# Optimization experiments

Measured on AMD Instinct MI355X. Metric: run time of the kernel, lower is better.

The kernel has to match this reference:

```python
import jax, jax.numpy as jnp
import numpy as np

EMBED = 512
WINDOW = 64

def setup_inputs() -> dict:
    key = jax.random.key(0)
    ks = jax.random.split(key, 5)
    B, S, E = 4, 4096, EMBED
    s = 1.0 / np.sqrt(E)
    x = jax.random.normal(ks[0], (B, S, E), dtype=jnp.float32)
    W_qkv = jax.random.uniform(ks[1], (E, 3 * E), minval=-s, maxval=s, dtype=jnp.float32)
    b_qkv = jax.random.uniform(ks[2], (3 * E,), minval=-s, maxval=s, dtype=jnp.float32)
    W_out = jax.random.uniform(ks[3], (E, E), minval=-s, maxval=s, dtype=jnp.float32)
    b_out = jax.random.uniform(ks[4], (E,), minval=-s, maxval=s, dtype=jnp.float32)
    return {"x": x, "W_qkv": W_qkv, "b_qkv": b_qkv, "W_out": W_out, "b_out": b_out}

def reference(x, W_qkv, b_qkv, W_out, b_out):
    B, S, E = x.shape
    scale = jnp.sqrt(jnp.asarray(E, dtype=x.dtype))
    qkv = x @ W_qkv + b_qkv                    # [B,S,3E]
    q, k, v = jnp.split(qkv, 3, axis=-1)       # each [B,S,E]
    scores = jnp.einsum('bqe,bke->bqk', q, k) / scale  # [B,S,S]
    pos = jnp.arange(S)
    dist = pos[None, :] - pos[:, None]         # [S,S]
    window_mask = jnp.abs(dist) <= WINDOW
    neg_inf = jnp.asarray(-jnp.inf, dtype=scores.dtype)
    scores = jnp.where(window_mask[None, :, :], scores, neg_inf)
    attn = jax.nn.softmax(scores, axis=-1)     # every row has in-window entries
    attended = jnp.einsum('bqk,bke->bqe', attn, v)
    return attended @ W_out + b_out
```

## Files before the change

### kernel.cpp

```cpp
#include <hip/hip_runtime.h>

typedef __attribute__((ext_vector_type(8))) _Float16 f16x8;
typedef __attribute__((ext_vector_type(4))) _Float16 f16x4;
typedef __attribute__((ext_vector_type(4))) float f32x4;
typedef __attribute__((address_space(1))) const char gc_char;
typedef __attribute__((address_space(3))) char ls_char;

#define MFMA(a, b, c) __builtin_amdgcn_mfma_f32_16x16x32_f16((a), (b), (c), 0, 0, 0)
#define FENCE() asm volatile("" ::: "memory")
#define BARRIER() do { FENCE(); __builtin_amdgcn_s_barrier(); FENCE(); } while (0)
#define VMW(n) asm volatile("s_waitcnt vmcnt(" #n ")" ::: "memory")

static constexpr int SEQ = 4096;
static constexpr int EMB = 512;
static constexpr float QSCALE = 0.04419417382415922f;

__device__ __forceinline__ void gl_lds16(const void* g, void* l) {
    __builtin_amdgcn_global_load_lds((gc_char*)g, (ls_char*)l, 16, 0, 0);
}

__global__ void k_prep(const float* __restrict__ x, _Float16* __restrict__ xb,
                       const float* __restrict__ Wq, _Float16* __restrict__ WqT,
                       const float* __restrict__ Wo, _Float16* __restrict__ WoT) {
    const int bid = blockIdx.x, tid = threadIdx.x;
    if (bid < 4096) {
        long i = (long)bid * 256 + tid;
        const float4* p = (const float4*)x + i * 2;
        float4 a = p[0], b = p[1];
        f16x8 v;
        v[0] = (_Float16)a.x; v[1] = (_Float16)a.y; v[2] = (_Float16)a.z; v[3] = (_Float16)a.w;
        v[4] = (_Float16)b.x; v[5] = (_Float16)b.y; v[6] = (_Float16)b.z; v[7] = (_Float16)b.w;
        *(f16x8*)(xb + i * 8) = v;
    } else {
        __shared__ float Ls[64][65];
        int t = bid - 4096;
        const float* W; _Float16* WT; int N, k0, n0;
        if (t < 192) { W = Wq; WT = WqT; N = 1536; k0 = (t & 7) * 64; n0 = (t >> 3) * 64; }
        else { t -= 192; W = Wo; WT = WoT; N = 512; k0 = (t & 7) * 64; n0 = (t >> 3) * 64; }
        int c = tid & 63, r4 = tid >> 6;
#pragma unroll
        for (int i = 0; i < 16; ++i) {
            int row = i * 4 + r4;
            Ls[row][c] = W[(long)(k0 + row) * N + n0 + c];
        }
        __syncthreads();
#pragma unroll
        for (int i = 0; i < 16; ++i) {
            int row = i * 4 + r4;
            WT[(long)(n0 + row) * 512 + k0 + c] = (_Float16)Ls[c][row];
        }
    }
}

__launch_bounds__(512, 1) __global__
void k_gemm_qkv(const _Float16* __restrict__ A, const _Float16* __restrict__ BT,
                const float* __restrict__ bias,
                _Float16* __restrict__ Qo, _Float16* __restrict__ Ko, _Float16* __restrict__ VT) {
    extern __shared__ __align__(16) char smem[];
    const int tid = threadIdx.x, lane = tid & 63, w = tid >> 6, g = lane >> 4, f = lane & 15;
    const int wrow = w >> 2, wcol = w & 3;
    const int bid = blockIdx.x;
    const int swz = (bid & 7) * 96 + (bid >> 3);
    const int brow = swz / 6, bcol = swz - brow * 6;
    const long row0 = (long)brow * 128;
    const int col0 = bcol * 256;
    const char* Abase = (const char*)A + row0 * 1024;
    const char* Bbase = (const char*)BT + (long)col0 * 1024;

    f32x4 acc[4][4] = {};
    f16x8 a[2][2], breg[2][2][2];

    auto stageA = [&](int h, char* dst, int kt) {
        int rr = tid >> 3;
        int ch = (tid & 7) ^ (rr & 7);
        int grow = h * 32 + (rr & 31) + (rr >> 5) * 64;
        gl_lds16(Abase + (long)grow * 1024 + kt * 128 + ch * 16, dst + h * 8192 + tid * 16);
    };
    auto stageB = [&](int h, char* dst, int kt) {
#pragma unroll
        for (int it = 0; it < 2; ++it) {
            int s = it * 512 + tid;
            int cc = s >> 3;
            int ch = (s & 7) ^ (cc & 7);
            int gcol = h * 32 + (cc & 31) + (cc >> 5) * 64;
            gl_lds16(Bbase + (long)gcol * 1024 + kt * 128 + ch * 16,
                     dst + 16384 + h * 16384 + s * 16);
        }
    };
    auto ldA = [&](const char* buf, int mh) {
#pragma unroll
        for (int mi = 0; mi < 2; ++mi)
#pragma unroll
            for (int ks = 0; ks < 2; ++ks) {
                int rr = wrow * 32 + mi * 16 + f;
                int cl = ks * 4 + g;
                a[mi][ks] = *(const f16x8*)(buf + mh * 8192 + rr * 128 + ((cl ^ (rr & 7)) << 4));
            }
    };
    auto ldB = [&](const char* buf, int nh) {
#pragma unroll
        for (int ni = 0; ni < 2; ++ni)
#pragma unroll
            for (int ks = 0; ks < 2; ++ks) {
                int cc = wcol * 32 + ni * 16 + f;
                int cl = ks * 4 + g;
                breg[nh][ni][ks] =
                    *(const f16x8*)(buf + 16384 + nh * 16384 + cc * 128 + ((cl ^ (cc & 7)) << 4));
            }
    };
    auto mfma8 = [&](int mh, int nh) {
        __builtin_amdgcn_s_setprio(1);
#pragma unroll
        for (int mi = 0; mi < 2; ++mi)
#pragma unroll
            for (int ni = 0; ni < 2; ++ni)
#pragma unroll
                for (int ks = 0; ks < 2; ++ks)
                    acc[mh * 2 + mi][nh * 2 + ni] =
                        MFMA(a[mi][ks], breg[nh][ni][ks], acc[mh * 2 + mi][nh * 2 + ni]);
        __builtin_amdgcn_s_setprio(0);
    };

    stageB(0, smem, 0);
    stageA(0, smem, 0); stageA(1, smem, 0);
    stageB(1, smem, 0);
    VMW(3);
    BARRIER();

    for (int kt = 0; kt < 8; ++kt) {
        const char* cur = smem + (kt & 1) * 49152;
        char* nxt = smem + ((kt + 1) & 1) * 49152;
        const bool last = (kt == 7);
        ldA(cur, 0); ldB(cur, 0);
        if (!last) stageB(0, nxt, kt + 1);
        BARRIER();
        mfma8(0, 0);
        if (!last) { VMW(2); } else { VMW(0); }
        BARRIER();
        ldB(cur, 1);
        if (!last) { stageA(0, nxt, kt + 1); stageA(1, nxt, kt + 1); }
        BARRIER();
        mfma8(0, 1);
        BARRIER();
        ldA(cur, 1);
        if (!last) stageB(1, nxt, kt + 1);
        BARRIER();
        mfma8(1, 0);
        BARRIER();
        mfma8(1, 1);
        if (!last) { VMW(3); }
        BARRIER();
    }

    float bv[4];
#pragma unroll
    for (int ni = 0; ni < 4; ++ni) bv[ni] = bias[col0 + wcol * 64 + ni * 16 + f];

    if (col0 >= 1024) {
#pragma unroll
        for (int mi = 0; mi < 4; ++mi)
#pragma unroll
            for (int ni = 0; ni < 4; ++ni) {
                int r0 = wrow * 64 + mi * 16 + g * 4;
                int c = wcol * 64 + ni * 16 + f;
                f16x4 v4;
#pragma unroll
                for (int j = 0; j < 4; ++j) v4[j] = (_Float16)(acc[mi][ni][j] + bv[ni]);
                *(f16x4*)(smem + c * 256 + ((r0 * 2) ^ ((c & 7) << 4))) = v4;
            }
        __syncthreads();
        int bb = (int)(row0 >> 12);
        _Float16* vt = VT + ((long)bb * 512 + (col0 - 1024)) * 4096 + (row0 & 4095);
#pragma unroll
        for (int it = 0; it < 8; ++it) {
            int slot = it * 512 + tid;
            int e = slot >> 4, ch = slot & 15;
            f16x8 v = *(const f16x8*)(smem + e * 256 + ((ch * 16) ^ ((e & 7) << 4)));
            *(f16x8*)(vt + (long)e * 4096 + ch * 8) = v;
        }
    } else {
        const float sc = (col0 < 512) ? QSCALE : 1.0f;
#pragma unroll
        for (int mi = 0; mi < 4; ++mi)
#pragma unroll
            for (int ni = 0; ni < 4; ++ni)
#pragma unroll
                for (int j = 0; j < 4; ++j) {
                    int r = wrow * 64 + mi * 16 + g * 4 + j;
                    int c = wcol * 64 + ni * 16 + f;
                    float v = (acc[mi][ni][j] + bv[ni]) * sc;
                    int pc = ((c >> 3) + ((r >> 2) & 7) * 2) & 31;
                    *(_Float16*)(smem + r * 512 + pc * 16 + (c & 7) * 2) = (_Float16)v;
                }
        __syncthreads();
        _Float16* dst = (col0 < 512) ? Qo : Ko;
        int cofs = (col0 < 512) ? col0 : col0 - 512;
#pragma unroll
        for (int it = 0; it < 8; ++it) {
            int slot = it * 512 + tid;
            int r = slot >> 5, ch = slot & 31;
            int pc = (ch + ((r >> 2) & 7) * 2) & 31;
            f16x8 v = *(const f16x8*)(smem + r * 512 + pc * 16);
            *(f16x8*)(dst + (row0 + r) * 512 + cofs + ch * 8) = v;
        }
    }
}

__launch_bounds__(512, 1) __global__
void k_attn(const _Float16* __restrict__ Qb, const _Float16* __restrict__ Kb,
            const _Float16* __restrict__ VT, const _Float16* __restrict__ WoT,
            const float* __restrict__ bout, float* __restrict__ Out) {
    extern __shared__ __align__(16) char smem[];
    char* buf[2] = { smem, smem + 49152 };
    char* Pl = smem + 98304;
    float* Mp = (float*)(smem + 123904);
    float* Lp = (float*)(smem + 124928);

    const int tid = threadIdx.x, w = tid >> 6, lane = tid & 63, g = lane >> 4, f = lane & 15;
    const int rh = w >> 2, kh = w & 3;
    const int bid = blockIdx.x;
    const int swzb = (bid & 7) * 32 + (bid >> 3);
    const int b = swzb >> 6, qt = swzb & 63;
    const int q0 = qt * 64, kbase = q0 - 64;
    const long bofs = (long)b * SEQ;

    f16x8 qf[2][16];
#pragma unroll
    for (int mt = 0; mt < 2; ++mt) {
        const _Float16* qr = Qb + (bofs + q0 + rh * 32 + mt * 16 + f) * EMB + g * 8;
#pragma unroll
        for (int ks = 0; ks < 16; ++ks) qf[mt][ks] = *(const f16x8*)(qr + ks * 32);
    }

    auto stageK = [&](int ec, char* dst) {
#pragma unroll
        for (int it = 0; it < 6; ++it) {
            int slot = it * 512 + tid;
            int r = slot >> 4, c = slot & 15;
            int cs = c ^ (r & 7);
            int key = min(max(kbase + r, 0), SEQ - 1);
            gl_lds16(Kb + (bofs + key) * EMB + ec * 128 + cs * 8, dst + slot * 16);
        }
    };
    auto stageVT = [&](int ec, char* dst) {
#pragma unroll
        for (int it = 0; it < 6; ++it) {
            int slot = it * 512 + tid;
            int r = slot / 24, c = slot - r * 24;
            int cs = c ^ (r & 7);
            int k0 = min(max(kbase + cs * 8, 0), SEQ - 8);
            gl_lds16(VT + ((long)b * 512 + ec * 128 + r) * 4096 + k0, dst + slot * 16);
        }
    };

    f32x4 sacc[2][3] = {};
    stageK(0, buf[0]);
    __syncthreads();
    for (int ec = 0; ec < 4; ++ec) {
        if (ec < 3) stageK(ec + 1, buf[(ec + 1) & 1]);
        else stageVT(0, buf[0]);
        const char* kb = buf[ec & 1];
#pragma unroll
        for (int kk = 0; kk < 4; ++kk) {
#pragma unroll
            for (int t = 0; t < 3; ++t) {
                int n = kh * 48 + t * 16 + f;
                f16x8 bf = *(const f16x8*)(kb + n * 256 + (((kk * 4 + g) ^ (n & 7)) << 4));
#pragma unroll
                for (int mt = 0; mt < 2; ++mt)
                    sacc[mt][t] = MFMA(qf[mt][ec * 4 + kk], bf, sacc[mt][t]);
            }
        }
        __syncthreads();
    }

    float m[2][4] = {{-3e30f, -3e30f, -3e30f, -3e30f}, {-3e30f, -3e30f, -3e30f, -3e30f}};
    float l[2][4] = {};
#pragma unroll
    for (int mt = 0; mt < 2; ++mt)
#pragma unroll
        for (int t = 0; t < 3; ++t) {
            int key = kbase + kh * 48 + t * 16 + f;
            bool kv = (key >= 0) && (key < SEQ);
#pragma unroll
            for (int j = 0; j < 4; ++j) {
                int d = key - (q0 + rh * 32 + mt * 16 + g * 4 + j);
                bool valid = kv && (d >= -64) && (d <= 64);
                float s = valid ? sacc[mt][t][j] : -3e30f;
                sacc[mt][t][j] = s;
                m[mt][j] = fmaxf(m[mt][j], s);
            }
        }
#pragma unroll
    for (int mt = 0; mt < 2; ++mt)
#pragma unroll
        for (int j = 0; j < 4; ++j) {
            m[mt][j] = fmaxf(m[mt][j], __shfl_xor(m[mt][j], 1));
            m[mt][j] = fmaxf(m[mt][j], __shfl_xor(m[mt][j], 2));
            m[mt][j] = fmaxf(m[mt][j], __shfl_xor(m[mt][j], 4));
            m[mt][j] = fmaxf(m[mt][j], __shfl_xor(m[mt][j], 8));
        }
    if (f == 0) {
#pragma unroll
        for (int mt = 0; mt < 2; ++mt)
#pragma unroll
            for (int j = 0; j < 4; ++j)
                Mp[kh * 64 + rh * 32 + mt * 16 + g * 4 + j] = m[mt][j];
    }
    __syncthreads();
#pragma unroll
    for (int mt = 0; mt < 2; ++mt)
#pragma unroll
        for (int j = 0; j < 4; ++j) {
            int r = rh * 32 + mt * 16 + g * 4 + j;
            m[mt][j] = fmaxf(fmaxf(Mp[r], Mp[64 + r]), fmaxf(Mp[128 + r], Mp[192 + r]));
        }
#pragma unroll
    for (int mt = 0; mt < 2; ++mt)
#pragma unroll
        for (int t = 0; t < 3; ++t)
#pragma unroll
            for (int j = 0; j < 4; ++j) {
                float p = __expf(sacc[mt][t][j] - m[mt][j]);
                sacc[mt][t][j] = p;
                l[mt][j] += p;
            }
#pragma unroll
    for (int mt = 0; mt < 2; ++mt)
#pragma unroll
        for (int j = 0; j < 4; ++j) {
            l[mt][j] += __shfl_xor(l[mt][j], 1);
            l[mt][j] += __shfl_xor(l[mt][j], 2);
            l[mt][j] += __shfl_xor(l[mt][j], 4);
            l[mt][j] += __shfl_xor(l[mt][j], 8);
        }
    if (f == 0) {
#pragma unroll
        for (int mt = 0; mt < 2; ++mt)
#pragma unroll
            for (int j = 0; j < 4; ++j)
                Lp[kh * 64 + rh * 32 + mt * 16 + g * 4 + j] = l[mt][j];
    }
#pragma unroll
    for (int mt = 0; mt < 2; ++mt)
#pragma unroll
        for (int t = 0; t < 3; ++t)
#pragma unroll
            for (int j = 0; j < 4; ++j)
                *(_Float16*)(Pl + (rh * 32 + mt * 16 + g * 4 + j) * 400 +
                             (kh * 48 + t * 16 + f) * 2) = (_Float16)sacc[mt][t][j];
    __syncthreads();

    float rl[2][4];
#pragma unroll
    for (int mt = 0; mt < 2; ++mt)
#pragma unroll
        for (int j = 0; j < 4; ++j) {
            int r = rh * 32 + mt * 16 + g * 4 + j;
            rl[mt][j] = 1.0f / (Lp[r] + Lp[64 + r] + Lp[128 + r] + Lp[192 + r]);
        }

    f16x8 pf[2][6];
#pragma unroll
    for (int mt = 0; mt < 2; ++mt)
#pragma unroll
        for (int kc = 0; kc < 6; ++kc)
            pf[mt][kc] = *(const f16x8*)(Pl + (rh * 32 + mt * 16 + f) * 400 + kc * 64 + g * 16);

    f32x4 oacc[4][2][2] = {};
#pragma unroll
    for (int ec = 0; ec < 4; ++ec) {
        if (ec < 3) stageVT(ec + 1, buf[(ec + 1) & 1]);
        const char* vb = buf[ec & 1];
#pragma unroll
        for (int kc = 0; kc < 6; ++kc) {
#pragma unroll
            for (int nt = 0; nt < 2; ++nt) {
                int e = kh * 32 + nt * 16 + f;
                f16x8 vf = *(const f16x8*)(vb + e * 384 + (((kc * 4 + g) ^ (e & 7)) << 4));
#pragma unroll
                for (int mt = 0; mt < 2; ++mt)
                    oacc[ec][mt][nt] = MFMA(pf[mt][kc], vf, oacc[ec][mt][nt]);
            }
        }
        if (ec < 3) __syncthreads();
    }

    __syncthreads();
    char* att = smem;
    char* wb0 = smem + 65536;
    char* wb1 = smem + 98304;

    auto stageW = [&](int u, char* dst) {
#pragma unroll
        for (int i = 0; i < 4; ++i) {
            int s = i * 512 + tid;
            int col = s >> 2, ch = s & 3;
            gl_lds16(WoT + (long)col * 512 + u * 32 + ((ch ^ (col & 3)) * 8), dst + s * 16);
        }
    };
    stageW(0, wb0);
    stageW(1, wb1);
#pragma unroll
    for (int ec = 0; ec < 4; ++ec)
#pragma unroll
        for (int mt = 0; mt < 2; ++mt)
#pragma unroll
            for (int nt = 0; nt < 2; ++nt)
#pragma unroll
                for (int j = 0; j < 4; ++j) {
                    int row = rh * 32 + mt * 16 + g * 4 + j;
                    int col = ec * 128 + kh * 32 + nt * 16 + f;
                    *(_Float16*)(att + row * 1024 + ((col * 2) ^ ((row & 7) << 4))) =
                        (_Float16)(oacc[ec][mt][nt][j] * rl[mt][j]);
                }
    __syncthreads();

    float bv2[8];
#pragma unroll
    for (int nt = 0; nt < 8; ++nt) bv2[nt] = bout[kh * 128 + nt * 16 + f];

    f32x4 acc2[2][8] = {};
    for (int u = 0; u < 16; ++u) {
        const char* wcur = (u & 1) ? wb1 : wb0;
        f16x8 a2[2];
#pragma unroll
        for (int mt = 0; mt < 2; ++mt) {
            int row = rh * 32 + mt * 16 + f;
            a2[mt] = *(const f16x8*)(att + row * 1024 + ((u * 64 + g * 16) ^ ((row & 7) << 4)));
        }
        __builtin_amdgcn_s_setprio(1);
#pragma unroll
        for (int nt = 0; nt < 8; ++nt) {
            int col = kh * 128 + nt * 16 + f;
            f16x8 b2 = *(const f16x8*)(wcur + col * 64 + ((g * 16) ^ ((col & 3) << 4)));
#pragma unroll
            for (int mt = 0; mt < 2; ++mt)
                acc2[mt][nt] = MFMA(a2[mt], b2, acc2[mt][nt]);
        }
        __builtin_amdgcn_s_setprio(0);
        BARRIER();
        if (u + 2 < 16) {
            stageW(u + 2, (u & 1) ? wb1 : wb0);
            VMW(4);
        } else {
            VMW(0);
        }
        BARRIER();
    }

#pragma unroll
    for (int mt = 0; mt < 2; ++mt)
#pragma unroll
        for (int nt = 0; nt < 8; ++nt) {
            long r0 = bofs + q0 + rh * 32 + mt * 16 + g * 4;
            int c = kh * 128 + nt * 16 + f;
#pragma unroll
            for (int j = 0; j < 4; ++j)
                Out[(r0 + j) * 512 + c] = acc2[mt][nt][j] + bv2[nt];
        }
}

extern "C" void kernel_launch(void* const* d_in, const int* in_sizes, int n_in,
                              void* d_out, int out_size, void* d_ws, size_t ws_size,
                              hipStream_t stream) {
    const float* x     = (const float*)d_in[0];
    const float* W_qkv = (const float*)d_in[1];
    const float* b_qkv = (const float*)d_in[2];
    const float* W_out = (const float*)d_in[3];
    const float* b_out = (const float*)d_in[4];

    char* ws = (char*)d_ws;
    _Float16* xb    = (_Float16*)(ws);
    _Float16* WqkvT = (_Float16*)(ws + 16777216);
    _Float16* WoutT = (_Float16*)(ws + 16777216 + 1572864);
    _Float16* Qb    = (_Float16*)(ws + 18874368);
    _Float16* Kb    = (_Float16*)(ws + 18874368 + 16777216);
    _Float16* VT    = (_Float16*)(ws + 18874368 + 33554432);
    float* out = (float*)d_out;

    (void)hipFuncSetAttribute((const void*)k_gemm_qkv,
                              hipFuncAttributeMaxDynamicSharedMemorySize, 98304);
    (void)hipFuncSetAttribute((const void*)k_attn,
                              hipFuncAttributeMaxDynamicSharedMemorySize, 131072);

    k_prep<<<4352, 256, 0, stream>>>(x, xb, W_qkv, WqkvT, W_out, WoutT);
    k_gemm_qkv<<<768, 512, 98304, stream>>>(xb, WqkvT, b_qkv, Qb, Kb, VT);
    k_attn<<<256, 512, 131072, stream>>>(Qb, Kb, VT, WoutT, b_out, out);
}
```

Before: 80.50 us.

## Halve attention query tile to 32 rows, single-buffer LDS, raise occupancy

The attention kernel now handles 32 query rows per block instead of 64, launching 512 blocks with 64KB LDS and launch bounds allowing more resident blocks. Double buffering of the K, V^T and W_out tiles is replaced by a single buffer with barriers, and the key window shrinks to 160 keys. Idle key tiles are skipped per wave. The aim is better occupancy and less wasted window work, with reduced load/compute overlap inside a block and W_out reloaded by twice as many blocks in exchange.

```diff
diff --git a/kernel.cpp b/kernel.cpp
--- a/kernel.cpp
+++ b/kernel.cpp
@@ -206,259 +206,218 @@
     }
 }
 
-__launch_bounds__(512, 1) __global__
+__launch_bounds__(512, 4) __global__
 void k_attn(const _Float16* __restrict__ Qb, const _Float16* __restrict__ Kb,
             const _Float16* __restrict__ VT, const _Float16* __restrict__ WoT,
             const float* __restrict__ bout, float* __restrict__ Out) {
     extern __shared__ __align__(16) char smem[];
-    char* buf[2] = { smem, smem + 49152 };
-    char* Pl = smem + 98304;
-    float* Mp = (float*)(smem + 123904);
-    float* Lp = (float*)(smem + 124928);
+    char* buf = smem;
+    char* Pl = smem + 49152;
+    float* Mp = (float*)(smem + 59904);
+    float* Lp = (float*)(smem + 60416);
+    char* att = smem;
+    char* wbf = smem + 32768;
 
     const int tid = threadIdx.x, w = tid >> 6, lane = tid & 63, g = lane >> 4, f = lane & 15;
     const int rh = w >> 2, kh = w & 3;
+    const int NT = (kh < 2) ? 3 : 2;
     const int bid = blockIdx.x;
-    const int swzb = (bid & 7) * 32 + (bid >> 3);
-    const int b = swzb >> 6, qt = swzb & 63;
-    const int q0 = qt * 64, kbase = q0 - 64;
+    const int swzb = (bid & 7) * 64 + (bid >> 3);
+    const int b = swzb >> 7, qt = swzb & 127;
+    const int q0 = qt * 32, kbase = q0 - 64;
     const long bofs = (long)b * SEQ;
 
-    f16x8 qf[2][16];
-#pragma unroll
-    for (int mt = 0; mt < 2; ++mt) {
-        const _Float16* qr = Qb + (bofs + q0 + rh * 32 + mt * 16 + f) * EMB + g * 8;
-#pragma unroll
-        for (int ks = 0; ks < 16; ++ks) qf[mt][ks] = *(const f16x8*)(qr + ks * 32);
-    }
-
-    auto stageK = [&](int ec, char* dst) {
-#pragma unroll
-        for (int it = 0; it < 6; ++it) {
+    const _Float16* qr = Qb + (bofs + q0 + rh * 16 + f) * EMB;
+    f16x8 qf[16];
+#pragma unroll
+    for (int s = 0; s < 16; ++s) qf[s] = *(const f16x8*)(qr + s * 32 + g * 8);
+
+    auto stageK = [&](int ec) {
+#pragma unroll
+        for (int it = 0; it < 5; ++it) {
             int slot = it * 512 + tid;
             int r = slot >> 4, c = slot & 15;
             int cs = c ^ (r & 7);
             int key = min(max(kbase + r, 0), SEQ - 1);
-            gl_lds16(Kb + (bofs + key) * EMB + ec * 128 + cs * 8, dst + slot * 16);
-        }
-    };
-    auto stageVT = [&](int ec, char* dst) {
+            gl_lds16(Kb + (bofs + key) * EMB + ec * 128 + cs * 8, buf + slot * 16);
+        }
+    };
+    auto stageVT = [&](int ec) {
 #pragma unroll
         for (int it = 0; it < 6; ++it) {
             int slot = it * 512 + tid;
             int r = slot / 24, c = slot - r * 24;
             int cs = c ^ (r & 7);
             int k0 = min(max(kbase + cs * 8, 0), SEQ - 8);
-            gl_lds16(VT + ((long)b * 512 + ec * 128 + r) * 4096 + k0, dst + slot * 16);
-        }
-    };
-
-    f32x4 sacc[2][3] = {};
-    stageK(0, buf[0]);
+            gl_lds16(VT + ((long)b * 512 + ec * 128 + r) * 4096 + k0, buf + slot * 16);
+        }
+    };
+
+    f32x4 sacc[3] = {};
+    stageK(0);
     __syncthreads();
+#pragma unroll
     for (int ec = 0; ec < 4; ++ec) {
-        if (ec < 3) stageK(ec + 1, buf[(ec + 1) & 1]);
-        else stageVT(0, buf[0]);
-        const char* kb = buf[ec & 1];
 #pragma unroll
         for (int kk = 0; kk < 4; ++kk) {
 #pragma unroll
             for (int t = 0; t < 3; ++t) {
-                int n = kh * 48 + t * 16 + f;
-                f16x8 bf = *(const f16x8*)(kb + n * 256 + (((kk * 4 + g) ^ (n & 7)) << 4));
-#pragma unroll
-                for (int mt = 0; mt < 2; ++mt)
-                    sacc[mt][t] = MFMA(qf[mt][ec * 4 + kk], bf, sacc[mt][t]);
-            }
-        }
-        __syncthreads();
-    }
-
-    float m[2][4] = {{-3e30f, -3e30f, -3e30f, -3e30f}, {-3e30f, -3e30f, -3e30f, -3e30f}};
-    float l[2][4] = {};
-#pragma unroll
-    for (int mt = 0; mt < 2; ++mt)
-#pragma unroll
-        for (int t = 0; t < 3; ++t) {
-            int key = kbase + kh * 48 + t * 16 + f;
+                if (t < NT) {
+                    int n = (kh + t * 4) * 16 + f;
+                    f16x8 bf = *(const f16x8*)(buf + n * 256 + (((kk * 4 + g) ^ (n & 7)) << 4));
+                    sacc[t] = MFMA(qf[ec * 4 + kk], bf, sacc[t]);
+                }
+            }
+        }
+        __syncthreads();
+        if (ec < 3) { stageK(ec + 1); __syncthreads(); }
+    }
+
+    float m[4] = {-3e30f, -3e30f, -3e30f, -3e30f}, l[4] = {0.f, 0.f, 0.f, 0.f};
+#pragma unroll
+    for (int t = 0; t < 3; ++t) {
+        if (t < NT) {
+            int key = kbase + (kh + t * 4) * 16 + f;
             bool kv = (key >= 0) && (key < SEQ);
 #pragma unroll
             for (int j = 0; j < 4; ++j) {
-                int d = key - (q0 + rh * 32 + mt * 16 + g * 4 + j);
+                int d = key - (q0 + rh * 16 + g * 4 + j);
                 bool valid = kv && (d >= -64) && (d <= 64);
-                float s = valid ? sacc[mt][t][j] : -3e30f;
-                sacc[mt][t][j] = s;
-                m[mt][j] = fmaxf(m[mt][j], s);
-            }
-        }
-#pragma unroll
-    for (int mt = 0; mt < 2; ++mt)
-#pragma unroll
-        for (int j = 0; j < 4; ++j) {
-            m[mt][j] = fmaxf(m[mt][j], __shfl_xor(m[mt][j], 1));
-            m[mt][j] = fmaxf(m[mt][j], __shfl_xor(m[mt][j], 2));
-            m[mt][j] = fmaxf(m[mt][j], __shfl_xor(m[mt][j], 4));
-            m[mt][j] = fmaxf(m[mt][j], __shfl_xor(m[mt][j], 8));
-        }
+                float s = valid ? sacc[t][j] : -3e30f;
+                sacc[t][j] = s;
+                m[j] = fmaxf(m[j], s);
+            }
+        }
+    }
+#pragma unroll
+    for (int j = 0; j < 4; ++j) {
+        m[j] = fmaxf(m[j], __shfl_xor(m[j], 1));
+        m[j] = fmaxf(m[j], __shfl_xor(m[j], 2));
+        m[j] = fmaxf(m[j], __shfl_xor(m[j], 4));
+        m[j] = fmaxf(m[j], __shfl_xor(m[j], 8));
+    }
     if (f == 0) {
 #pragma unroll
-        for (int mt = 0; mt < 2; ++mt)
+        for (int j = 0; j < 4; ++j) Mp[kh * 32 + rh * 16 + g * 4 + j] = m[j];
+    }
+    __syncthreads();
+#pragma unroll
+    for (int j = 0; j < 4; ++j) {
+        int r = rh * 16 + g * 4 + j;
+        m[j] = fmaxf(fmaxf(Mp[r], Mp[32 + r]), fmaxf(Mp[64 + r], Mp[96 + r]));
+    }
+#pragma unroll
+    for (int t = 0; t < 3; ++t) {
+        if (t < NT) {
+#pragma unroll
+            for (int j = 0; j < 4; ++j) {
+                float p = __expf(sacc[t][j] - m[j]);
+                sacc[t][j] = p;
+                l[j] += p;
+            }
+        }
+    }
+#pragma unroll
+    for (int j = 0; j < 4; ++j) {
+        l[j] += __shfl_xor(l[j], 1);
+        l[j] += __shfl_xor(l[j], 2);
+        l[j] += __shfl_xor(l[j], 4);
+        l[j] += __shfl_xor(l[j], 8);
+    }
+    if (f == 0) {
+#pragma unroll
+        for (int j = 0; j < 4; ++j) Lp[kh * 32 + rh * 16 + g * 4 + j] = l[j];
+    }
+#pragma unroll
+    for (int t = 0; t < 3; ++t) {
+        if (t < NT) {
 #pragma unroll
             for (int j = 0; j < 4; ++j)
-                Mp[kh * 64 + rh * 32 + mt * 16 + g * 4 + j] = m[mt][j];
+                *(_Float16*)(Pl + (rh * 16 + g * 4 + j) * 336 +
+                             ((kh + t * 4) * 16 + f) * 2) = (_Float16)sacc[t][j];
+        }
     }
     __syncthreads();
-#pragma unroll
-    for (int mt = 0; mt < 2; ++mt)
-#pragma unroll
-        for (int j = 0; j < 4; ++j) {
-            int r = rh * 32 + mt * 16 + g * 4 + j;
-            m[mt][j] = fmaxf(fmaxf(Mp[r], Mp[64 + r]), fmaxf(Mp[128 + r], Mp[192 + r]));
-        }
-#pragma unroll
-    for (int mt = 0; mt < 2; ++mt)
-#pragma unroll
-        for (int t = 0; t < 3; ++t)
-#pragma unroll
-            for (int j = 0; j < 4; ++j) {
-                float p = __expf(sacc[mt][t][j] - m[mt][j]);
-                sacc[mt][t][j] = p;
-                l[mt][j] += p;
-            }
-#pragma unroll
-    for (int mt = 0; mt < 2; ++mt)
-#pragma unroll
-        for (int j = 0; j < 4; ++j) {
-            l[mt][j] += __shfl_xor(l[mt][j], 1);
-            l[mt][j] += __shfl_xor(l[mt][j], 2);
-            l[mt][j] += __shfl_xor(l[mt][j], 4);
-            l[mt][j] += __shfl_xor(l[mt][j], 8);
-        }
-    if (f == 0) {
-#pragma unroll
-        for (int mt = 0; mt < 2; ++mt)
-#pragma unroll
-            for (int j = 0; j < 4; ++j)
-                Lp[kh * 64 + rh * 32 + mt * 16 + g * 4 + j] = l[mt][j];
-    }
-#pragma unroll
-    for (int mt = 0; mt < 2; ++mt)
-#pragma unroll
-        for (int t = 0; t < 3; ++t)
-#pragma unroll
-            for (int j = 0; j < 4; ++j)
-                *(_Float16*)(Pl + (rh * 32 + mt * 16 + g * 4 + j) * 400 +
-                             (kh * 48 + t * 16 + f) * 2) = (_Float16)sacc[mt][t][j];
+    stageVT(0);
+
+    float rl[4];
+#pragma unroll
+    for (int j = 0; j < 4; ++j) {
+        int r = rh * 16 + g * 4 + j;
+        rl[j] = 1.0f / (Lp[r] + Lp[32 + r] + Lp[64 + r] + Lp[96 + r]);
+    }
+    f16x8 pf[5];
+#pragma unroll
+    for (int kc = 0; kc < 5; ++kc)
+        pf[kc] = *(const f16x8*)(Pl + (rh * 16 + f) * 336 + kc * 64 + g * 16);
     __syncthreads();
 
-    float rl[2][4];
-#pragma unroll
-    for (int mt = 0; mt < 2; ++mt)
-#pragma unroll
-        for (int j = 0; j < 4; ++j) {
-            int r = rh * 32 + mt * 16 + g * 4 + j;
-            rl[mt][j] = 1.0f / (Lp[r] + Lp[64 + r] + Lp[128 + r] + Lp[192 + r]);
-        }
-
-    f16x8 pf[2][6];
-#pragma unroll
-    for (int mt = 0; mt < 2; ++mt)
-#pragma unroll
-        for (int kc = 0; kc < 6; ++kc)
-            pf[mt][kc] = *(const f16x8*)(Pl + (rh * 32 + mt * 16 + f) * 400 + kc * 64 + g * 16);
-
-    f32x4 oacc[4][2][2] = {};
+    f32x4 oacc[4][2] = {};
 #pragma unroll
     for (int ec = 0; ec < 4; ++ec) {
-        if (ec < 3) stageVT(ec + 1, buf[(ec + 1) & 1]);
-        const char* vb = buf[ec & 1];
-#pragma unroll
-        for (int kc = 0; kc < 6; ++kc) {
+#pragma unroll
+        for (int kc = 0; kc < 5; ++kc) {
 #pragma unroll
             for (int nt = 0; nt < 2; ++nt) {
                 int e = kh * 32 + nt * 16 + f;
-                f16x8 vf = *(const f16x8*)(vb + e * 384 + (((kc * 4 + g) ^ (e & 7)) << 4));
-#pragma unroll
-                for (int mt = 0; mt < 2; ++mt)
-                    oacc[ec][mt][nt] = MFMA(pf[mt][kc], vf, oacc[ec][mt][nt]);
-            }
-        }
-        if (ec < 3) __syncthreads();
-    }
-
-    __syncthreads();
-    char* att = smem;
-    char* wb0 = smem + 65536;
-    char* wb1 = smem + 98304;
-
-    auto stageW = [&](int u, char* dst) {
+                f16x8 vf = *(const f16x8*)(buf + e * 384 + (((kc * 4 + g) ^ (e & 7)) << 4));
+                oacc[ec][nt] = MFMA(pf[kc], vf, oacc[ec][nt]);
+            }
+        }
+        __syncthreads();
+        if (ec < 3) { stageVT(ec + 1); __syncthreads(); }
+    }
+
+    auto stageW = [&](int u) {
 #pragma unroll
         for (int i = 0; i < 4; ++i) {
             int s = i * 512 + tid;
             int col = s >> 2, ch = s & 3;
-            gl_lds16(WoT + (long)col * 512 + u * 32 + ((ch ^ (col & 3)) * 8), dst + s * 16);
-        }
-    };
-    stageW(0, wb0);
-    stageW(1, wb1);
+            gl_lds16(WoT + (long)col * 512 + u * 32 + ((ch ^ (col & 3)) * 8), wbf + s * 16);
+        }
+    };
 #pragma unroll
     for (int ec = 0; ec < 4; ++ec)
 #pragma unroll
-        for (int mt = 0; mt < 2; ++mt)
-#pragma unroll
-            for (int nt = 0; nt < 2; ++nt)
-#pragma unroll
-                for (int j = 0; j < 4; ++j) {
-                    int row = rh * 32 + mt * 16 + g * 4 + j;
-                    int col = ec * 128 + kh * 32 + nt * 16 + f;
-                    *(_Float16*)(att + row * 1024 + ((col * 2) ^ ((row & 7) << 4))) =
-                        (_Float16)(oacc[ec][mt][nt][j] * rl[mt][j]);
-                }
+        for (int nt = 0; nt < 2; ++nt)
+#pragma unroll
+            for (int j = 0; j < 4; ++j) {
+                int row = rh * 16 + g * 4 + j;
+                int col = ec * 128 + kh * 32 + nt * 16 + f;
+                *(_Float16*)(att + row * 1024 + ((col * 2) ^ ((row & 7) << 4))) =
+                    (_Float16)(oacc[ec][nt][j] * rl[j]);
+            }
+    stageW(0);
     __syncthreads();
 
     float bv2[8];
 #pragma unroll
     for (int nt = 0; nt < 8; ++nt) bv2[nt] = bout[kh * 128 + nt * 16 + f];
 
-    f32x4 acc2[2][8] = {};
+    f32x4 acc2[8] = {};
     for (int u = 0; u < 16; ++u) {
-        const char* wcur = (u & 1) ? wb1 : wb0;
-        f16x8 a2[2];
-#pragma unroll
-        for (int mt = 0; mt < 2; ++mt) {
-            int row = rh * 32 + mt * 16 + f;
-            a2[mt] = *(const f16x8*)(att + row * 1024 + ((u * 64 + g * 16) ^ ((row & 7) << 4)));
-        }
+        int arow = rh * 16 + f;
+        f16x8 a2 = *(const f16x8*)(att + arow * 1024 + ((u * 64 + g * 16) ^ ((arow & 7) << 4)));
         __builtin_amdgcn_s_setprio(1);
 #pragma unroll
         for (int nt = 0; nt < 8; ++nt) {
             int col = kh * 128 + nt * 16 + f;
-            f16x8 b2 = *(const f16x8*)(wcur + col * 64 + ((g * 16) ^ ((col & 3) << 4)));
-#pragma unroll
-            for (int mt = 0; mt < 2; ++mt)
-                acc2[mt][nt] = MFMA(a2[mt], b2, acc2[mt][nt]);
+            f16x8 b2 = *(const f16x8*)(wbf + col * 64 + ((g * 16) ^ ((col & 3) << 4)));
+            acc2[nt] = MFMA(a2, b2, acc2[nt]);
         }
         __builtin_amdgcn_s_setprio(0);
-        BARRIER();
-        if (u + 2 < 16) {
-            stageW(u + 2, (u & 1) ? wb1 : wb0);
-            VMW(4);
-        } else {
-            VMW(0);
-        }
-        BARRIER();
-    }
-
-#pragma unroll
-    for (int mt = 0; mt < 2; ++mt)
-#pragma unroll
-        for (int nt = 0; nt < 8; ++nt) {
-            long r0 = bofs + q0 + rh * 32 + mt * 16 + g * 4;
-            int c = kh * 128 + nt * 16 + f;
-#pragma unroll
-            for (int j = 0; j < 4; ++j)
-                Out[(r0 + j) * 512 + c] = acc2[mt][nt][j] + bv2[nt];
-        }
+        __syncthreads();
+        if (u < 15) { stageW(u + 1); __syncthreads(); }
+    }
+
+#pragma unroll
+    for (int nt = 0; nt < 8; ++nt) {
+        long r0 = bofs + q0 + rh * 16 + g * 4;
+        int c = kh * 128 + nt * 16 + f;
+#pragma unroll
+        for (int j = 0; j < 4; ++j)
+            Out[(r0 + j) * 512 + c] = acc2[nt][j] + bv2[nt];
+    }
 }
 
 extern "C" void kernel_launch(void* const* d_in, const int* in_sizes, int n_in,
@@ -482,9 +441,9 @@
     (void)hipFuncSetAttribute((const void*)k_gemm_qkv,
                               hipFuncAttributeMaxDynamicSharedMemorySize, 98304);
     (void)hipFuncSetAttribute((const void*)k_attn,
-                              hipFuncAttributeMaxDynamicSharedMemorySize, 131072);
+                              hipFuncAttributeMaxDynamicSharedMemorySize, 65536);
 
     k_prep<<<4352, 256, 0, stream>>>(x, xb, W_qkv, WqkvT, W_out, WoutT);
     k_gemm_qkv<<<768, 512, 98304, stream>>>(xb, WqkvT, b_qkv, Qb, Kb, VT);
-    k_attn<<<256, 512, 131072, stream>>>(Qb, Kb, VT, WoutT, b_out, out);
+    k_attn<<<512, 512, 65536, stream>>>(Qb, Kb, VT, WoutT, b_out, out);
 }
```

After: 86.66 us. 1.08x slower.

## Fuse fp32-to-fp16 conversion of x into QKV GEMM A-tile loading

Applied to the files above, without the earlier changes.

Removes the separate pass that converts x to fp16 in the prep kernel. The QKV GEMM now loads fp32 x into registers, converts it, and writes swizzled fp16 tiles to LDS, with the pipeline waits adjusted to match. The out-projection weight staging also switches to a simpler unswizzled LDS layout. This saves a full read and write of x, but A-loads now pass through registers instead of direct-to-LDS loads and read twice as many bytes per tile. The new W layout may add LDS bank conflicts.

```diff
diff --git a/kernel.cpp b/kernel.cpp
--- a/kernel.cpp
+++ b/kernel.cpp
@@ -10,6 +10,7 @@
 #define FENCE() asm volatile("" ::: "memory")
 #define BARRIER() do { FENCE(); __builtin_amdgcn_s_barrier(); FENCE(); } while (0)
 #define VMW(n) asm volatile("s_waitcnt vmcnt(" #n ")" ::: "memory")
+#define LGW() asm volatile("s_waitcnt lgkmcnt(0)" ::: "memory")
 
 static constexpr int SEQ = 4096;
 static constexpr int EMB = 512;
@@ -19,41 +20,30 @@
     __builtin_amdgcn_global_load_lds((gc_char*)g, (ls_char*)l, 16, 0, 0);
 }
 
-__global__ void k_prep(const float* __restrict__ x, _Float16* __restrict__ xb,
-                       const float* __restrict__ Wq, _Float16* __restrict__ WqT,
+__global__ void k_prep(const float* __restrict__ Wq, _Float16* __restrict__ WqT,
                        const float* __restrict__ Wo, _Float16* __restrict__ WoT) {
-    const int bid = blockIdx.x, tid = threadIdx.x;
-    if (bid < 4096) {
-        long i = (long)bid * 256 + tid;
-        const float4* p = (const float4*)x + i * 2;
-        float4 a = p[0], b = p[1];
-        f16x8 v;
-        v[0] = (_Float16)a.x; v[1] = (_Float16)a.y; v[2] = (_Float16)a.z; v[3] = (_Float16)a.w;
-        v[4] = (_Float16)b.x; v[5] = (_Float16)b.y; v[6] = (_Float16)b.z; v[7] = (_Float16)b.w;
-        *(f16x8*)(xb + i * 8) = v;
-    } else {
-        __shared__ float Ls[64][65];
-        int t = bid - 4096;
-        const float* W; _Float16* WT; int N, k0, n0;
-        if (t < 192) { W = Wq; WT = WqT; N = 1536; k0 = (t & 7) * 64; n0 = (t >> 3) * 64; }
-        else { t -= 192; W = Wo; WT = WoT; N = 512; k0 = (t & 7) * 64; n0 = (t >> 3) * 64; }
-        int c = tid & 63, r4 = tid >> 6;
-#pragma unroll
-        for (int i = 0; i < 16; ++i) {
-            int row = i * 4 + r4;
-            Ls[row][c] = W[(long)(k0 + row) * N + n0 + c];
-        }
-        __syncthreads();
-#pragma unroll
-        for (int i = 0; i < 16; ++i) {
-            int row = i * 4 + r4;
-            WT[(long)(n0 + row) * 512 + k0 + c] = (_Float16)Ls[c][row];
-        }
+    __shared__ float Ls[64][65];
+    const int tid = threadIdx.x;
+    int t = blockIdx.x;
+    const float* W; _Float16* WT; int N, k0, n0;
+    if (t < 192) { W = Wq; WT = WqT; N = 1536; k0 = (t & 7) * 64; n0 = (t >> 3) * 64; }
+    else { t -= 192; W = Wo; WT = WoT; N = 512; k0 = (t & 7) * 64; n0 = (t >> 3) * 64; }
+    int c = tid & 63, r4 = tid >> 6;
+#pragma unroll
+    for (int i = 0; i < 16; ++i) {
+        int row = i * 4 + r4;
+        Ls[row][c] = W[(long)(k0 + row) * N + n0 + c];
+    }
+    __syncthreads();
+#pragma unroll
+    for (int i = 0; i < 16; ++i) {
+        int row = i * 4 + r4;
+        WT[(long)(n0 + row) * 512 + k0 + c] = (_Float16)Ls[c][row];
     }
 }
 
 __launch_bounds__(512, 1) __global__
-void k_gemm_qkv(const _Float16* __restrict__ A, const _Float16* __restrict__ BT,
+void k_gemm_qkv(const float* __restrict__ xg, const _Float16* __restrict__ BT,
                 const float* __restrict__ bias,
                 _Float16* __restrict__ Qo, _Float16* __restrict__ Ko, _Float16* __restrict__ VT) {
     extern __shared__ __align__(16) char smem[];
@@ -64,17 +54,38 @@
     const int brow = swz / 6, bcol = swz - brow * 6;
     const long row0 = (long)brow * 128;
     const int col0 = bcol * 256;
-    const char* Abase = (const char*)A + row0 * 1024;
+    const char* Abase32 = (const char*)xg + row0 * 2048;
     const char* Bbase = (const char*)BT + (long)col0 * 1024;
 
     f32x4 acc[4][4] = {};
     f16x8 a[2][2], breg[2][2][2];
-
-    auto stageA = [&](int h, char* dst, int kt) {
-        int rr = tid >> 3;
-        int ch = (tid & 7) ^ (rr & 7);
-        int grow = h * 32 + (rr & 31) + (rr >> 5) * 64;
-        gl_lds16(Abase + (long)grow * 1024 + kt * 128 + ch * 16, dst + h * 8192 + tid * 16);
+    float4 areg[4];
+
+    auto loadA = [&](int kt) {
+#pragma unroll
+        for (int c = 0; c < 2; ++c) {
+            int s = c * 512 + tid;
+            int lrr = s >> 3, cl = s & 7;
+            int rr = lrr & 63, mh = lrr >> 6;
+            int grow = mh * 32 + (rr & 31) + (rr >> 5) * 64;
+            const float4* src =
+                (const float4*)(Abase32 + (long)grow * 2048 + kt * 256 + cl * 32);
+            areg[c * 2] = src[0];
+            areg[c * 2 + 1] = src[1];
+        }
+    };
+    auto writeA = [&](char* dstbuf) {
+#pragma unroll
+        for (int c = 0; c < 2; ++c) {
+            int s = c * 512 + tid;
+            int lrr = s >> 3, cl = s & 7;
+            f16x8 v;
+            v[0] = (_Float16)areg[c * 2].x; v[1] = (_Float16)areg[c * 2].y;
+            v[2] = (_Float16)areg[c * 2].z; v[3] = (_Float16)areg[c * 2].w;
+            v[4] = (_Float16)areg[c * 2 + 1].x; v[5] = (_Float16)areg[c * 2 + 1].y;
+            v[6] = (_Float16)areg[c * 2 + 1].z; v[7] = (_Float16)areg[c * 2 + 1].w;
+            *(f16x8*)(dstbuf + lrr * 128 + ((cl ^ (lrr & 7)) << 4)) = v;
+        }
     };
     auto stageB = [&](int h, char* dst, int kt) {
 #pragma unroll
@@ -121,24 +132,26 @@
         __builtin_amdgcn_s_setprio(0);
     };
 
+    loadA(0);
     stageB(0, smem, 0);
-    stageA(0, smem, 0); stageA(1, smem, 0);
     stageB(1, smem, 0);
-    VMW(3);
+    writeA(smem);
+    VMW(2);
+    LGW();
     BARRIER();
 
     for (int kt = 0; kt < 8; ++kt) {
-        const char* cur = smem + (kt & 1) * 49152;
+        char* cur = smem + (kt & 1) * 49152;
         char* nxt = smem + ((kt + 1) & 1) * 49152;
         const bool last = (kt == 7);
         ldA(cur, 0); ldB(cur, 0);
-        if (!last) stageB(0, nxt, kt + 1);
+        if (!last) { loadA(kt + 1); stageB(0, nxt, kt + 1); }
         BARRIER();
         mfma8(0, 0);
-        if (!last) { VMW(2); } else { VMW(0); }
+        if (!last) { VMW(10); } else { VMW(0); }
         BARRIER();
         ldB(cur, 1);
-        if (!last) { stageA(0, nxt, kt + 1); stageA(1, nxt, kt + 1); }
+        if (!last) writeA(nxt);
         BARRIER();
         mfma8(0, 1);
         BARRIER();
@@ -148,7 +161,7 @@
         mfma8(1, 0);
         BARRIER();
         mfma8(1, 1);
-        if (!last) { VMW(3); }
+        if (!last) { VMW(2); LGW(); }
         BARRIER();
     }
 
@@ -395,8 +408,7 @@
 #pragma unroll
         for (int i = 0; i < 4; ++i) {
             int s = i * 512 + tid;
-            int col = s >> 2, ch = s & 3;
-            gl_lds16(WoT + (long)col * 512 + u * 32 + ((ch ^ (col & 3)) * 8), dst + s * 16);
+            gl_lds16(WoT + (long)tid * 512 + u * 32 + i * 8, dst + s * 16);
         }
     };
     stageW(0, wb0);
@@ -433,7 +445,7 @@
 #pragma unroll
         for (int nt = 0; nt < 8; ++nt) {
             int col = kh * 128 + nt * 16 + f;
-            f16x8 b2 = *(const f16x8*)(wcur + col * 64 + ((g * 16) ^ ((col & 3) << 4)));
+            f16x8 b2 = *(const f16x8*)(wcur + g * 8192 + col * 16);
 #pragma unroll
             for (int mt = 0; mt < 2; ++mt)
                 acc2[mt][nt] = MFMA(a2[mt], b2, acc2[mt][nt]);
@@ -471,7 +483,6 @@
     const float* b_out = (const float*)d_in[4];
 
     char* ws = (char*)d_ws;
-    _Float16* xb    = (_Float16*)(ws);
     _Float16* WqkvT = (_Float16*)(ws + 16777216);
     _Float16* WoutT = (_Float16*)(ws + 16777216 + 1572864);
     _Float16* Qb    = (_Float16*)(ws + 18874368);
@@ -484,7 +495,7 @@
     (void)hipFuncSetAttribute((const void*)k_attn,
                               hipFuncAttributeMaxDynamicSharedMemorySize, 131072);
 
-    k_prep<<<4352, 256, 0, stream>>>(x, xb, W_qkv, WqkvT, W_out, WoutT);
-    k_gemm_qkv<<<768, 512, 98304, stream>>>(xb, WqkvT, b_qkv, Qb, Kb, VT);
+    k_prep<<<256, 256, 0, stream>>>(W_qkv, WqkvT, W_out, WoutT);
+    k_gemm_qkv<<<768, 512, 98304, stream>>>(x, WqkvT, b_qkv, Qb, Kb, VT);
     k_attn<<<256, 512, 131072, stream>>>(Qb, Kb, VT, WoutT, b_out, out);
 }
```

Result: slower. 101.3 us (+25.9%).
